# Performance work log

Hardware: AMD Instinct MI355X
Metric: run time of the kernel (lower is better)

The kernel has to match this reference:

```python
import jax, jax.numpy as jnp
import numpy as np

CODEBOOK_SIZE = 8192
CODEBOOK_DIM = 1024
HIDDEN_DIM = 4096
OUT_DIM = 1024
B, M = 32, 576


def setup_inputs() -> dict:
    key = jax.random.key(0)
    k_idx, k_cb, k_w1, k_w2 = jax.random.split(key, 4)
    index = jax.random.randint(k_idx, (B, M), 0, CODEBOOK_SIZE, dtype=jnp.int32)
    # codebook initialized as sqrt(d) * randn, as in the torch module
    codebook = (CODEBOOK_DIM ** 0.5) * jax.random.normal(k_cb, (CODEBOOK_SIZE, CODEBOOK_DIM), dtype=jnp.float32)
    s1 = 1.0 / np.sqrt(CODEBOOK_DIM)
    s2 = 1.0 / np.sqrt(HIDDEN_DIM)
    W1 = s1 * jax.random.normal(k_w1, (CODEBOOK_DIM, HIDDEN_DIM), dtype=jnp.float32)
    b1 = jnp.zeros((HIDDEN_DIM,), dtype=jnp.float32)
    W2 = s2 * jax.random.normal(k_w2, (HIDDEN_DIM, OUT_DIM), dtype=jnp.float32)
    b2 = jnp.zeros((OUT_DIM,), dtype=jnp.float32)
    return {"index": index, "codebook": codebook, "W1": W1, "b1": b1, "W2": W2, "b2": b2}


def reference(index, codebook, W1, b1, W2, b2):
    # one_hot(index) @ codebook is mathematically an index gather:
    # quantized[b, m, :] = codebook[index[b, m], :]
    quantized = jnp.take(codebook, index, axis=0)  # [B, M, D]
    # Decoder_ff: 2-layer GELU MLP (D -> 4D -> D)
    h = jax.nn.gelu(jnp.einsum('bmd,dh->bmh', quantized, W1) + b1)
    rec = jnp.einsum('bmh,ho->bmo', h, W2) + b2
    return rec
```

## Files before the change

### kernel.cpp

```cpp
#include <hip/hip_runtime.h>
#include <stdint.h>

typedef __attribute__((ext_vector_type(8))) short s16x8;
typedef __attribute__((ext_vector_type(4))) float f32x4;

__device__ __forceinline__ short f2bf(float x) {
  uint32_t u = __builtin_bit_cast(uint32_t, x);
  u += 0x7FFFu + ((u >> 16) & 1u);
  return (short)(u >> 16);
}

__device__ __forceinline__ void gload16(void* l, const void* g) {
  __builtin_amdgcn_global_load_lds(
      (const __attribute__((address_space(1))) void*)g,
      (__attribute__((address_space(3))) void*)l, 16, 0, 0);
}

__device__ __forceinline__ float gelu_tanh(float x) {
  float u = 0.7978845608028654f * (x + 0.044715f * x * x * x);
  float e = __expf(2.0f * u);
  return x - x / (e + 1.0f);
}

__global__ void gather_cvt(const float* __restrict__ cb, const int* __restrict__ idx,
                           short* __restrict__ out) {
  int m = blockIdx.x * 2 + (threadIdx.x >> 7);
  int c = (threadIdx.x & 127) * 8;
  const float* s = cb + (size_t)idx[m] * 1024 + c;
  s16x8 o;
#pragma unroll
  for (int j = 0; j < 8; ++j) o[j] = f2bf(s[j]);
  *(s16x8*)(out + (size_t)m * 1024 + c) = o;
}

__global__ void cvt_T(const float* __restrict__ in, short* __restrict__ out, int K, int N) {
  int Kb = K >> 3;
  int t = blockIdx.x * 256 + threadIdx.x;
  if (t >= N * Kb) return;
  int n = t / Kb;
  int k8 = (t - n * Kb) * 8;
  const float* s = in + (size_t)k8 * N + n;
  s16x8 o;
#pragma unroll
  for (int j = 0; j < 8; ++j) o[j] = f2bf(s[(size_t)j * N]);
  *(s16x8*)(out + (size_t)n * K + k8) = o;
}

template <int MODE, int K, int N>
__global__ __launch_bounds__(512, 2) void gemmk(
    const short* __restrict__ A, const short* __restrict__ Bt,
    const float* __restrict__ bias, void* __restrict__ Cv) {
  constexpr int BM = 192, BN = 256;
  constexpr int AHS = BM * 64;
  constexpr int BHS = BN * 64;
  constexpr int BB = 2 * AHS;
  __shared__ short lds[2 * AHS + 3 * BHS];

  constexpr int NBN = N / BN;
  const int nwg = gridDim.x;
  int swz = blockIdx.x;
  swz = (swz & 7) * (nwg >> 3) + (swz >> 3);
  const int bm = swz / NBN, bn = swz - (swz / NBN) * NBN;

  const int tid = threadIdx.x;
  const int wid = tid >> 6, lane = tid & 63;
  const int wr = wid >> 2, wc = wid & 3;
  const int lr = lane & 15, hi = lane >> 4;

  const int sl = (tid & 7) ^ ((tid >> 3) & 7);
  const long rstep = (long)64 * K;
  const short* aptr = A + (long)(bm * BM + (tid >> 3)) * K + sl * 8;
  const short* bptr = Bt + (long)(bn * BN + (tid >> 3)) * K + sl * 8;
  const int wlds = wid * 512;

  const int aRB = (wr * 96 + lr) * 64;
  const int bRB = (wc * 64 + lr) * 64;
  const int sk0 = (hi ^ (lr & 7)) * 8;
  const int sk1 = ((4 + hi) ^ (lr & 7)) * 8;

  f32x4 acc[6][4] = {};
  s16x8 af[3][2], bf[4][2];

  constexpr int NT = K >> 6;

#pragma unroll
  for (int r = 0; r < 3; ++r) gload16(&lds[r * 4096 + wlds], aptr + r * rstep);
#pragma unroll
  for (int r = 0; r < 4; ++r) gload16(&lds[BB + r * 4096 + wlds], bptr + r * rstep);
#pragma unroll
  for (int r = 0; r < 4; ++r) gload16(&lds[BB + BHS + r * 4096 + wlds], bptr + r * rstep + 64);
  asm volatile("s_waitcnt vmcnt(4)" ::: "memory");
  __builtin_amdgcn_s_barrier();

  int rb0 = BB, rb1 = BB + BHS, rb2 = BB + 2 * BHS;

  for (int t = 0; t < NT; ++t) {
    const int ca = (t & 1) * AHS;
    const int na = AHS - ca;
    const int ka = ((t + 1 < NT) ? (t + 1) : t) << 6;
    const int kb = ((t + 2 < NT) ? (t + 2) : t) << 6;

#pragma unroll
    for (int r = 0; r < 3; ++r) gload16(&lds[na + r * 4096 + wlds], aptr + r * rstep + ka);

#pragma unroll
    for (int mi = 0; mi < 3; ++mi) {
      af[mi][0] = *(const s16x8*)&lds[ca + aRB + mi * 1024 + sk0];
      af[mi][1] = *(const s16x8*)&lds[ca + aRB + mi * 1024 + sk1];
    }
#pragma unroll
    for (int nj = 0; nj < 4; ++nj) {
      bf[nj][0] = *(const s16x8*)&lds[rb0 + bRB + nj * 1024 + sk0];
      bf[nj][1] = *(const s16x8*)&lds[rb0 + bRB + nj * 1024 + sk1];
    }
    asm volatile("s_waitcnt lgkmcnt(0)" ::: "memory");
    __builtin_amdgcn_s_setprio(1);
#pragma unroll
    for (int mi = 0; mi < 3; ++mi)
#pragma unroll
      for (int nj = 0; nj < 4; ++nj)
#pragma unroll
        for (int ks = 0; ks < 2; ++ks)
          acc[mi][nj] = __builtin_amdgcn_mfma_f32_16x16x32_bf16(af[mi][ks], bf[nj][ks], acc[mi][nj], 0, 0, 0);
    __builtin_amdgcn_s_setprio(0);

#pragma unroll
    for (int r = 0; r < 4; ++r)
      gload16(&lds[rb2 + r * 4096 + wlds], bptr + r * rstep + kb);
#pragma unroll
    for (int mi = 0; mi < 3; ++mi) {
      af[mi][0] = *(const s16x8*)&lds[ca + aRB + (3 + mi) * 1024 + sk0];
      af[mi][1] = *(const s16x8*)&lds[ca + aRB + (3 + mi) * 1024 + sk1];
    }
    asm volatile("s_waitcnt lgkmcnt(0)" ::: "memory");
    __builtin_amdgcn_s_setprio(1);
#pragma unroll
    for (int mi = 0; mi < 3; ++mi)
#pragma unroll
      for (int nj = 0; nj < 4; ++nj)
#pragma unroll
        for (int ks = 0; ks < 2; ++ks)
          acc[3 + mi][nj] = __builtin_amdgcn_mfma_f32_16x16x32_bf16(af[mi][ks], bf[nj][ks], acc[3 + mi][nj], 0, 0, 0);
    __builtin_amdgcn_s_setprio(0);

    asm volatile("s_waitcnt vmcnt(4)" ::: "memory");
    __builtin_amdgcn_s_barrier();
    const int tmp = rb0; rb0 = rb1; rb1 = rb2; rb2 = tmp;
  }

  const int m0 = bm * BM + wr * 96 + hi * 4;
  const int n0 = bn * BN + wc * 64 + lr;
#pragma unroll
  for (int nj = 0; nj < 4; ++nj) {
    const int n = n0 + nj * 16;
    const float bv = bias[n];
#pragma unroll
    for (int mi = 0; mi < 6; ++mi) {
      f32x4 v = acc[mi][nj];
#pragma unroll
      for (int r = 0; r < 4; ++r) {
        const int m = m0 + mi * 16 + r;
        float x = v[r] + bv;
        if (MODE == 1) {
          ((short*)Cv)[(size_t)m * N + n] = f2bf(gelu_tanh(x));
        } else {
          ((float*)Cv)[(size_t)m * N + n] = x;
        }
      }
    }
  }
}

extern "C" void kernel_launch(void* const* d_in, const int* in_sizes, int n_in,
                              void* d_out, int out_size, void* d_ws, size_t ws_size,
                              hipStream_t stream) {
  const int* idx = (const int*)d_in[0];
  const float* cb = (const float*)d_in[1];
  const float* W1 = (const float*)d_in[2];
  const float* b1 = (const float*)d_in[3];
  const float* W2 = (const float*)d_in[4];
  const float* b2 = (const float*)d_in[5];
  float* out = (float*)d_out;

  const int Mtot = 32 * 576;

  char* ws = (char*)d_ws;
  short* aq = (short*)(ws);
  short* w1t = (short*)(ws + (size_t)40 * 1024 * 1024);
  short* w2t = (short*)(ws + (size_t)48 * 1024 * 1024);
  short* h = (short*)(ws + (size_t)56 * 1024 * 1024);

  gather_cvt<<<Mtot / 2, 256, 0, stream>>>(cb, idx, aq);
  cvt_T<<<2048, 256, 0, stream>>>(W1, w1t, 1024, 4096);
  cvt_T<<<2048, 256, 0, stream>>>(W2, w2t, 4096, 1024);

  size_t avail = (ws_size > (size_t)56 * 1024 * 1024) ? ws_size - (size_t)56 * 1024 * 1024 : 0;
  int nc = 1;
  while (nc < 8 && (size_t)(Mtot / nc) * 8192 > avail) nc <<= 1;
  const int Mc = Mtot / nc;

  for (int c = 0; c < nc; ++c) {
    gemmk<1, 1024, 4096><<<(Mc / 192) * 16, 512, 0, stream>>>(
        aq + (size_t)c * Mc * 1024, w1t, b1, (void*)h);
    gemmk<2, 4096, 1024><<<(Mc / 192) * 4, 512, 0, stream>>>(
        h, w2t, b2, (void*)(out + (size_t)c * Mc * 1024));
  }
}
```

Before: 436.3 us.

## Split GEMM main loop into four MFMA phases with interleaved loads and barriers

The GEMM k-loop's two MFMA clusters are split into four smaller clusters over half of the B fragments each. The global-to-LDS prefetches for the next A tile and the tile-after-next B tile are spread across these phases instead of being issued in two bursts. Workgroup barriers are inserted around each phase so waves issue memory and MFMA work in lockstep, aiming to overlap load issue with matrix math more evenly. The extra barriers add synchronisation cost and may reduce the latency hiding that independent wave scheduling gave before.

```diff
diff --git a/kernel.cpp b/kernel.cpp
--- a/kernel.cpp
+++ b/kernel.cpp
@@ -47,7 +47,7 @@
 }
 
 template <int MODE, int K, int N>
-__global__ __launch_bounds__(512, 2) void gemmk(
+__global__ __launch_bounds__(512, 2) void gemmq(
     const short* __restrict__ A, const short* __restrict__ Bt,
     const float* __restrict__ bias, void* __restrict__ Cv) {
   constexpr int BM = 192, BN = 256;
@@ -79,7 +79,7 @@
   const int sk1 = ((4 + hi) ^ (lr & 7)) * 8;
 
   f32x4 acc[6][4] = {};
-  s16x8 af[3][2], bf[4][2];
+  s16x8 af[3][2], bf0[2][2], bf1[2][2];
 
   constexpr int NT = K >> 6;
 
@@ -101,48 +101,80 @@
     const int kb = ((t + 2 < NT) ? (t + 2) : t) << 6;
 
 #pragma unroll
-    for (int r = 0; r < 3; ++r) gload16(&lds[na + r * 4096 + wlds], aptr + r * rstep + ka);
-
-#pragma unroll
     for (int mi = 0; mi < 3; ++mi) {
       af[mi][0] = *(const s16x8*)&lds[ca + aRB + mi * 1024 + sk0];
       af[mi][1] = *(const s16x8*)&lds[ca + aRB + mi * 1024 + sk1];
     }
 #pragma unroll
-    for (int nj = 0; nj < 4; ++nj) {
-      bf[nj][0] = *(const s16x8*)&lds[rb0 + bRB + nj * 1024 + sk0];
-      bf[nj][1] = *(const s16x8*)&lds[rb0 + bRB + nj * 1024 + sk1];
-    }
+    for (int nj = 0; nj < 2; ++nj) {
+      bf0[nj][0] = *(const s16x8*)&lds[rb0 + bRB + nj * 1024 + sk0];
+      bf0[nj][1] = *(const s16x8*)&lds[rb0 + bRB + nj * 1024 + sk1];
+    }
+    gload16(&lds[na + 0 * 4096 + wlds], aptr + 0 * rstep + ka);
+    gload16(&lds[na + 1 * 4096 + wlds], aptr + 1 * rstep + ka);
+    __builtin_amdgcn_s_barrier();
     asm volatile("s_waitcnt lgkmcnt(0)" ::: "memory");
     __builtin_amdgcn_s_setprio(1);
 #pragma unroll
     for (int mi = 0; mi < 3; ++mi)
 #pragma unroll
-      for (int nj = 0; nj < 4; ++nj)
-#pragma unroll
-        for (int ks = 0; ks < 2; ++ks)
-          acc[mi][nj] = __builtin_amdgcn_mfma_f32_16x16x32_bf16(af[mi][ks], bf[nj][ks], acc[mi][nj], 0, 0, 0);
-    __builtin_amdgcn_s_setprio(0);
-
-#pragma unroll
-    for (int r = 0; r < 4; ++r)
-      gload16(&lds[rb2 + r * 4096 + wlds], bptr + r * rstep + kb);
+      for (int nj = 0; nj < 2; ++nj)
+#pragma unroll
+        for (int ks = 0; ks < 2; ++ks)
+          acc[mi][nj] = __builtin_amdgcn_mfma_f32_16x16x32_bf16(af[mi][ks], bf0[nj][ks], acc[mi][nj], 0, 0, 0);
+    __builtin_amdgcn_s_setprio(0);
+    __builtin_amdgcn_s_barrier();
+
+#pragma unroll
+    for (int nj = 0; nj < 2; ++nj) {
+      bf1[nj][0] = *(const s16x8*)&lds[rb0 + bRB + (2 + nj) * 1024 + sk0];
+      bf1[nj][1] = *(const s16x8*)&lds[rb0 + bRB + (2 + nj) * 1024 + sk1];
+    }
+    gload16(&lds[na + 2 * 4096 + wlds], aptr + 2 * rstep + ka);
+    gload16(&lds[rb2 + 0 * 4096 + wlds], bptr + 0 * rstep + kb);
+    __builtin_amdgcn_s_barrier();
+    asm volatile("s_waitcnt lgkmcnt(0)" ::: "memory");
+    __builtin_amdgcn_s_setprio(1);
+#pragma unroll
+    for (int mi = 0; mi < 3; ++mi)
+#pragma unroll
+      for (int nj = 0; nj < 2; ++nj)
+#pragma unroll
+        for (int ks = 0; ks < 2; ++ks)
+          acc[mi][2 + nj] = __builtin_amdgcn_mfma_f32_16x16x32_bf16(af[mi][ks], bf1[nj][ks], acc[mi][2 + nj], 0, 0, 0);
+    __builtin_amdgcn_s_setprio(0);
+    __builtin_amdgcn_s_barrier();
+
 #pragma unroll
     for (int mi = 0; mi < 3; ++mi) {
       af[mi][0] = *(const s16x8*)&lds[ca + aRB + (3 + mi) * 1024 + sk0];
       af[mi][1] = *(const s16x8*)&lds[ca + aRB + (3 + mi) * 1024 + sk1];
     }
+    gload16(&lds[rb2 + 1 * 4096 + wlds], bptr + 1 * rstep + kb);
+    gload16(&lds[rb2 + 2 * 4096 + wlds], bptr + 2 * rstep + kb);
+    __builtin_amdgcn_s_barrier();
     asm volatile("s_waitcnt lgkmcnt(0)" ::: "memory");
     __builtin_amdgcn_s_setprio(1);
 #pragma unroll
     for (int mi = 0; mi < 3; ++mi)
 #pragma unroll
-      for (int nj = 0; nj < 4; ++nj)
-#pragma unroll
-        for (int ks = 0; ks < 2; ++ks)
-          acc[3 + mi][nj] = __builtin_amdgcn_mfma_f32_16x16x32_bf16(af[mi][ks], bf[nj][ks], acc[3 + mi][nj], 0, 0, 0);
-    __builtin_amdgcn_s_setprio(0);
-
+      for (int nj = 0; nj < 2; ++nj)
+#pragma unroll
+        for (int ks = 0; ks < 2; ++ks)
+          acc[3 + mi][nj] = __builtin_amdgcn_mfma_f32_16x16x32_bf16(af[mi][ks], bf0[nj][ks], acc[3 + mi][nj], 0, 0, 0);
+    __builtin_amdgcn_s_setprio(0);
+    __builtin_amdgcn_s_barrier();
+
+    gload16(&lds[rb2 + 3 * 4096 + wlds], bptr + 3 * rstep + kb);
+    __builtin_amdgcn_s_setprio(1);
+#pragma unroll
+    for (int mi = 0; mi < 3; ++mi)
+#pragma unroll
+      for (int nj = 0; nj < 2; ++nj)
+#pragma unroll
+        for (int ks = 0; ks < 2; ++ks)
+          acc[3 + mi][2 + nj] = __builtin_amdgcn_mfma_f32_16x16x32_bf16(af[mi][ks], bf1[nj][ks], acc[3 + mi][2 + nj], 0, 0, 0);
+    __builtin_amdgcn_s_setprio(0);
     asm volatile("s_waitcnt vmcnt(4)" ::: "memory");
     __builtin_amdgcn_s_barrier();
     const int tmp = rb0; rb0 = rb1; rb1 = rb2; rb2 = tmp;
@@ -200,9 +232,9 @@
   const int Mc = Mtot / nc;
 
   for (int c = 0; c < nc; ++c) {
-    gemmk<1, 1024, 4096><<<(Mc / 192) * 16, 512, 0, stream>>>(
+    gemmq<1, 1024, 4096><<<(Mc / 192) * 16, 512, 0, stream>>>(
         aq + (size_t)c * Mc * 1024, w1t, b1, (void*)h);
-    gemmk<2, 4096, 1024><<<(Mc / 192) * 4, 512, 0, stream>>>(
+    gemmq<2, 4096, 1024><<<(Mc / 192) * 4, 512, 0, stream>>>(
         h, w2t, b2, (void*)(out + (size_t)c * Mc * 1024));
   }
 }
```

After: 446.4 us (median of 2 runs). 2.3% more time.
